# Kernel tuning notes

Measured on AMD Instinct MI355X. Metric: run time of the kernel, lower is better.

The kernel has to match this reference:

```python
import jax, jax.numpy as jnp
import numpy as np

SIMILARITY_EPS = 1e-4
B, N, M, K = 4096, 16384, 12, 2048  # batch, signal length, n ref spectra, spectrum bins


def setup_inputs() -> dict:
    key = jax.random.key(0)
    k1, k2, k3 = jax.random.split(key, 3)
    Y = jax.random.normal(k1, (B, N), dtype=jnp.float32)
    model_spectra = jax.random.uniform(k2, (M, K), dtype=jnp.float32)
    dissonance_vals = jax.random.uniform(k3, (M,), dtype=jnp.float32)
    return {"Y": Y, "model_spectra": model_spectra, "dissonance_vals": dissonance_vals}


def reference(Y, model_spectra, dissonance_vals):
    n = Y.shape[-1]
    k = model_spectra.shape[-1]
    # FFT magnitude spectrum, scaled, truncated to first K bins: [B, K]
    yf = (2.0 / n) * jnp.abs(jnp.fft.fft(Y, axis=-1)[:, :k])
    # Euclidean distance to each reference spectrum via expansion (avoids [B,M,K] intermediate)
    sq = (jnp.sum(yf * yf, axis=-1, keepdims=True)            # [B,1]
          + jnp.sum(model_spectra * model_spectra, axis=-1)   # [M]
          - 2.0 * (yf @ model_spectra.T))                     # [B,M]
    dist = jnp.sqrt(jnp.maximum(sq, 0.0))                     # [B,M]
    sim = 1.0 / (dist + SIMILARITY_EPS)                       # [B,M]
    w = sim / jnp.sum(sim, axis=-1, keepdims=True)            # [B,M]
    out = w @ (1.0 - dissonance_vals)                         # [B]
    return out[:, None]                                       # [B,1]
```

## Files before the change

### kernel.cpp

```cpp
#include <hip/hip_runtime.h>
#include <hip/hip_bf16.h>
#include <math.h>

#define BATCH 4096
#define NSIG  16384
#define MREF  12
#define KBIN  2048

constexpr float SIM_EPS = 1e-4f;
constexpr float TWO_PI = 6.2831853071795864769f;

typedef __attribute__((ext_vector_type(8))) short bfrag;
typedef __attribute__((ext_vector_type(4))) float f32x4;
typedef __attribute__((ext_vector_type(4))) int   i32x4;
typedef __attribute__((ext_vector_type(4))) unsigned u32x4;

__device__ unsigned g_wtab[16 * 256 * 4];
__device__ unsigned g_b2tab[1024 * 4];
__device__ unsigned g_utw[32 * 128 * 4];
__device__ float    g_msn[MREF];

__device__ inline unsigned short f2bf(float x) {
  unsigned u = __builtin_bit_cast(unsigned, x);
  u += 0x7fffu + ((u >> 16) & 1u);
  return (unsigned short)(u >> 16);
}
__device__ inline unsigned pkbf(float lo, float hi) {
  return (unsigned)f2bf(lo) | ((unsigned)f2bf(hi) << 16);
}
__device__ inline float bflo(unsigned u) { return __builtin_bit_cast(float, u << 16); }
__device__ inline float bfhi(unsigned u) { return __builtin_bit_cast(float, u & 0xffff0000u); }
__device__ inline f32x4 mfma16(bfrag a, bfrag b, f32x4 c) {
  return __builtin_amdgcn_mfma_f32_16x16x32_bf16(a, b, c, 0, 0, 0);
}

__global__ __launch_bounds__(256) void setup_kernel(const float* __restrict__ ms) {
  const int blk = blockIdx.x, t = threadIdx.x;
  if (blk < 16) {
    const int ri = blk & 1, ks = (blk >> 1) & 3, mt = blk >> 3;
    const int lane = t & 63, w = t >> 6, c = lane & 15, g = lane >> 4;
    const int k1 = 32 * w + 16 * mt + c;
    unsigned wd[4];
    #pragma unroll
    for (int jp = 0; jp < 4; ++jp) {
      float v[2];
      #pragma unroll
      for (int h = 0; h < 2; ++h) {
        const int n1 = 32 * ks + 8 * g + 2 * jp + h;
        const float th = TWO_PI * (float)((k1 * n1) & 127) / 128.f;
        float sn, cs; sincosf(th, &sn, &cs);
        v[h] = ri ? -sn : cs;
      }
      wd[jp] = pkbf(v[0], v[1]);
    }
    *(u32x4*)&g_wtab[(blk * 256 + t) * 4] = (u32x4){wd[0], wd[1], wd[2], wd[3]};
  } else if (blk == 16) {
    #pragma unroll
    for (int r = 0; r < 4; ++r) {
      const int e = t * 4 + r;
      const int lane = e & 63, ri = (e >> 6) & 1, s_ = (e >> 7) & 1, ch = (e >> 8) & 3;
      const int c = lane & 15, g = lane >> 4;
      unsigned wd[4];
      #pragma unroll
      for (int i = 0; i < 4; ++i) {
        const int ang = (c * (32 * ch + 16 * s_ + 4 * g + i)) & 127;
        const float th = TWO_PI * (float)ang / 128.f;
        float sn, cs; sincosf(th, &sn, &cs);
        wd[i] = ri ? pkbf(-sn, cs) : pkbf(cs, sn);
      }
      *(u32x4*)&g_b2tab[e * 4] = (u32x4){wd[0], wd[1], wd[2], wd[3]};
    }
  } else if (blk < 25) {
    const int base = (blk - 17) * 512 + t;
    #pragma unroll
    for (int r = 0; r < 2; ++r) {
      const int e = base + r * 256;
      const int a = e >> 7, n2 = e & 127;
      unsigned wd[4];
      #pragma unroll
      for (int q = 0; q < 4; ++q) {
        const int ang = ((4 * a + q) * n2) & 16383;
        const float th = TWO_PI * (float)ang / 16384.f;
        float sn, cs; sincosf(th, &sn, &cs);
        wd[q] = pkbf(cs, -sn);
      }
      *(u32x4*)&g_utw[e * 4] = (u32x4){wd[0], wd[1], wd[2], wd[3]};
    }
  } else {
    const int m = blk - 25;
    if (m < MREF) {
      float p = 0.f;
      for (int i = t; i < KBIN; i += 256) { float v = ms[m * KBIN + i]; p += v * v; }
      #pragma unroll
      for (int o = 32; o; o >>= 1) p += __shfl_xor(p, o, 64);
      __shared__ float r4[4];
      if ((t & 63) == 0) r4[t >> 6] = p;
      __syncthreads();
      if (t == 0) g_msn[m] = r4[0] + r4[1] + r4[2] + r4[3];
    }
  }
}

__global__ __launch_bounds__(256, 2) void consonance_kernel(
    const float* __restrict__ Y, const float* __restrict__ ms,
    const float* __restrict__ diss, float* __restrict__ out) {
  __shared__ __align__(16) unsigned short Ysb[128 * 128];
  __shared__ __align__(16) unsigned Ua[4 * 32 * 32];
  __shared__ float red[4][13];

  const int t = threadIdx.x;
  const int b = blockIdx.x;
  const int lane = t & 63;
  const int w = t >> 6;
  const int g = lane >> 4;
  const int c = lane & 15;

  {
    const int c0 = (t & 31) << 2;
    const int h  = t >> 5;
    const float* yrow = Y + (size_t)b * NSIG + c0;
    float4 v[16];
    #pragma unroll
    for (int r = 0; r < 16; ++r)
      v[r] = *(const float4*)(yrow + 128 * (16 * h + r));
    #pragma unroll
    for (int u = 0; u < 2; ++u) {
      #pragma unroll
      for (int cc = 0; cc < 4; ++cc) {
        const int n2 = c0 + cc;
        unsigned p0 = pkbf((&v[8*u+0].x)[cc], (&v[8*u+1].x)[cc]);
        unsigned p1 = pkbf((&v[8*u+2].x)[cc], (&v[8*u+3].x)[cc]);
        unsigned p2 = pkbf((&v[8*u+4].x)[cc], (&v[8*u+5].x)[cc]);
        unsigned p3 = pkbf((&v[8*u+6].x)[cc], (&v[8*u+7].x)[cc]);
        const int blk = (2 * h + u) ^ (n2 & 7);
        *(i32x4*)((char*)Ysb + n2 * 256 + (blk << 4)) =
            (i32x4){(int)p0, (int)p1, (int)p2, (int)p3};
      }
    }
  }

  bfrag Wr[2][4], Wi[2][4];
  #pragma unroll
  for (int mt = 0; mt < 2; ++mt)
    #pragma unroll
    for (int ks = 0; ks < 4; ++ks) {
      Wr[mt][ks] = *(const bfrag*)&g_wtab[(((mt * 4 + ks) * 2 + 0) * 256 + t) * 4];
      Wi[mt][ks] = *(const bfrag*)&g_wtab[(((mt * 4 + ks) * 2 + 1) * 256 + t) * 4];
    }

  f32x4 aXr[2] = {{0.f,0.f,0.f,0.f},{0.f,0.f,0.f,0.f}};
  f32x4 aXi[2] = {{0.f,0.f,0.f,0.f},{0.f,0.f,0.f,0.f}};
  unsigned* uw = Ua + (w << 10);

  __syncthreads();

  #pragma unroll 1
  for (int ch = 0; ch < 4; ++ch) {
    bfrag bfr[2][4];
    #pragma unroll
    for (int nt = 0; nt < 2; ++nt) {
      const int n2 = 32 * ch + 16 * nt + c;
      #pragma unroll
      for (int ks = 0; ks < 4; ++ks) {
        const int blk = (4 * ks + g) ^ (n2 & 7);
        bfr[nt][ks] = *(const bfrag*)((const char*)Ysb + n2 * 256 + (blk << 4));
      }
    }
    f32x4 aTr[2][2] = {{{0.f,0.f,0.f,0.f},{0.f,0.f,0.f,0.f}},
                       {{0.f,0.f,0.f,0.f},{0.f,0.f,0.f,0.f}}};
    f32x4 aTi[2][2] = {{{0.f,0.f,0.f,0.f},{0.f,0.f,0.f,0.f}},
                       {{0.f,0.f,0.f,0.f},{0.f,0.f,0.f,0.f}}};
    #pragma unroll
    for (int mt = 0; mt < 2; ++mt)
      #pragma unroll
      for (int nt = 0; nt < 2; ++nt)
        #pragma unroll
        for (int ks = 0; ks < 4; ++ks) {
          aTr[mt][nt] = mfma16(Wr[mt][ks], bfr[nt][ks], aTr[mt][nt]);
          aTi[mt][nt] = mfma16(Wi[mt][ks], bfr[nt][ks], aTi[mt][nt]);
        }
    #pragma unroll
    for (int nt = 0; nt < 2; ++nt) {
      const int n2 = 32 * ch + 16 * nt + c;
      #pragma unroll
      for (int mt = 0; mt < 2; ++mt) {
        const int a = 8 * w + 4 * mt + g;
        const u32x4 tw = *(const u32x4*)&g_utw[(a * 128 + n2) * 4];
        #pragma unroll
        for (int q = 0; q < 4; ++q) {
          const float twr = bflo(tw[q]), twi = bfhi(tw[q]);
          const float tr = aTr[mt][nt][q], ti = aTi[mt][nt][q];
          const float ur = tr * twr - ti * twi;
          const float ui = tr * twi + ti * twr;
          const int rl = 16 * mt + 4 * g + q;
          const int tt = 16 * nt + c;
          uw[rl * 32 + (tt ^ ((rl & 7) << 2))] = pkbf(ur, ui);
        }
      }
    }
    bfrag B2[2][2];
    #pragma unroll
    for (int s = 0; s < 2; ++s) {
      B2[0][s] = *(const bfrag*)&g_b2tab[(((ch * 2 + s) * 2 + 0) * 64 + lane) * 4];
      B2[1][s] = *(const bfrag*)&g_b2tab[(((ch * 2 + s) * 2 + 1) * 64 + lane) * 4];
    }
    #pragma unroll
    for (int mt = 0; mt < 2; ++mt) {
      const int rl = 16 * mt + c;
      #pragma unroll
      for (int s = 0; s < 2; ++s) {
        const int t4 = (16 * s + 4 * g) ^ ((rl & 7) << 2);
        bfrag af = *(const bfrag*)((const char*)uw + rl * 128 + (t4 << 2));
        aXr[mt] = mfma16(af, B2[0][s], aXr[mt]);
        aXi[mt] = mfma16(af, B2[1][s], aXi[mt]);
      }
    }
  }

  const float scale = 2.0f / (float)NSIG;
  float yfv[2][4], S = 0.f;
  #pragma unroll
  for (int mt = 0; mt < 2; ++mt)
    #pragma unroll
    for (int q = 0; q < 4; ++q) {
      const float xr = aXr[mt][q], xi = aXi[mt][q];
      const float yf = scale * sqrtf(xr * xr + xi * xi);
      yfv[mt][q] = yf;
      S += yf * yf;
    }
  float dot[MREF];
  #pragma unroll
  for (int m = 0; m < MREF; ++m) dot[m] = 0.f;
  const int kb0 = 32 * w + 4 * g + 128 * c;
  #pragma unroll
  for (int m = 0; m < MREF; ++m) {
    #pragma unroll
    for (int mt = 0; mt < 2; ++mt) {
      const float4 mv = *(const float4*)&ms[m * KBIN + kb0 + 16 * mt];
      dot[m] = fmaf(yfv[mt][0], mv.x, dot[m]);
      dot[m] = fmaf(yfv[mt][1], mv.y, dot[m]);
      dot[m] = fmaf(yfv[mt][2], mv.z, dot[m]);
      dot[m] = fmaf(yfv[mt][3], mv.w, dot[m]);
    }
  }
  #pragma unroll
  for (int o = 32; o; o >>= 1) {
    S += __shfl_xor(S, o, 64);
    #pragma unroll
    for (int m = 0; m < MREF; ++m) dot[m] += __shfl_xor(dot[m], o, 64);
  }
  if (lane == 0) {
    red[w][0] = S;
    #pragma unroll
    for (int m = 0; m < MREF; ++m) red[w][1 + m] = dot[m];
  }
  __syncthreads();
  if (t == 0) {
    const float St = red[0][0] + red[1][0] + red[2][0] + red[3][0];
    float ssum = 0.f, wsum = 0.f;
    for (int m = 0; m < MREF; ++m) {
      const float dm = red[0][1 + m] + red[1][1 + m] + red[2][1 + m] + red[3][1 + m];
      const float d2 = St + g_msn[m] - 2.f * dm;
      const float dist = sqrtf(fmaxf(d2, 0.f));
      const float sim = 1.f / (dist + SIM_EPS);
      ssum += sim;
      wsum += sim * (1.f - diss[m]);
    }
    out[b] = wsum / ssum;
  }
}

extern "C" void kernel_launch(void* const* d_in, const int* in_sizes, int n_in,
                              void* d_out, int out_size, void* d_ws, size_t ws_size,
                              hipStream_t stream) {
  const float* Y    = (const float*)d_in[0];
  const float* ms   = (const float*)d_in[1];
  const float* diss = (const float*)d_in[2];
  float* outp = (float*)d_out;
  setup_kernel<<<37, 256, 0, stream>>>(ms);
  consonance_kernel<<<BATCH, 256, 0, stream>>>(Y, ms, diss, outp);
}
```

Before: 435.8 us.

## Prefetch twiddles, use hardware bf16 pack, raise occupancy, fix LDS swizzle

Switches bf16 packing to the v_cvt_pk_bf16_f32 instruction instead of manual rounding. It raises launch bounds to 4 blocks per CU and splits the Y load into two halves to cut register pressure. Twiddle and W table loads are hoisted and software-prefetched one chunk ahead, and the chunk loop is fully unrolled. The LDS swizzle now mixes in higher row bits to reduce bank conflicts. Forcing 4 waves/SIMD may cause register spills, and the LDS footprint (~49KB per block) may cap occupancy anyway.

```diff
diff --git a/kernel.cpp b/kernel.cpp
--- a/kernel.cpp
+++ b/kernel.cpp
@@ -20,19 +20,17 @@
 __device__ unsigned g_utw[32 * 128 * 4];
 __device__ float    g_msn[MREF];
 
-__device__ inline unsigned short f2bf(float x) {
-  unsigned u = __builtin_bit_cast(unsigned, x);
-  u += 0x7fffu + ((u >> 16) & 1u);
-  return (unsigned short)(u >> 16);
-}
 __device__ inline unsigned pkbf(float lo, float hi) {
-  return (unsigned)f2bf(lo) | ((unsigned)f2bf(hi) << 16);
+  unsigned r;
+  asm("v_cvt_pk_bf16_f32 %0, %1, %2" : "=v"(r) : "v"(lo), "v"(hi));
+  return r;
 }
 __device__ inline float bflo(unsigned u) { return __builtin_bit_cast(float, u << 16); }
 __device__ inline float bfhi(unsigned u) { return __builtin_bit_cast(float, u & 0xffff0000u); }
 __device__ inline f32x4 mfma16(bfrag a, bfrag b, f32x4 c) {
   return __builtin_amdgcn_mfma_f32_16x16x32_bf16(a, b, c, 0, 0, 0);
 }
+__device__ inline int fsw(int n2) { return (n2 ^ (n2 >> 2)) & 7; }
 
 __global__ __launch_bounds__(256) void setup_kernel(const float* __restrict__ ms) {
   const int blk = blockIdx.x, t = threadIdx.x;
@@ -101,7 +99,7 @@
   }
 }
 
-__global__ __launch_bounds__(256, 2) void consonance_kernel(
+__global__ __launch_bounds__(256, 4) void consonance_kernel(
     const float* __restrict__ Y, const float* __restrict__ ms,
     const float* __restrict__ diss, float* __restrict__ out) {
   __shared__ __align__(16) unsigned short Ysb[128 * 128];
@@ -115,38 +113,46 @@
   const int g = lane >> 4;
   const int c = lane & 15;
 
+  bfrag Wr[2][4], Wi[2][4];
+  #pragma unroll
+  for (int mt = 0; mt < 2; ++mt)
+    #pragma unroll
+    for (int ks = 0; ks < 4; ++ks) {
+      Wr[mt][ks] = *(const bfrag*)&g_wtab[(((mt * 4 + ks) * 2 + 0) * 256 + t) * 4];
+      Wi[mt][ks] = *(const bfrag*)&g_wtab[(((mt * 4 + ks) * 2 + 1) * 256 + t) * 4];
+    }
+  u32x4 utwP[2][2];
+  #pragma unroll
+  for (int nt = 0; nt < 2; ++nt)
+    #pragma unroll
+    for (int mt = 0; mt < 2; ++mt) {
+      const int a = 8 * w + 4 * mt + g;
+      utwP[nt][mt] = *(const u32x4*)&g_utw[(a * 128 + (16 * nt + c)) * 4];
+    }
+
   {
     const int c0 = (t & 31) << 2;
     const int h  = t >> 5;
     const float* yrow = Y + (size_t)b * NSIG + c0;
-    float4 v[16];
-    #pragma unroll
-    for (int r = 0; r < 16; ++r)
-      v[r] = *(const float4*)(yrow + 128 * (16 * h + r));
     #pragma unroll
     for (int u = 0; u < 2; ++u) {
+      float4 v[8];
+      #pragma unroll
+      for (int r = 0; r < 8; ++r)
+        v[r] = *(const float4*)(yrow + 128 * (16 * h + 8 * u + r));
       #pragma unroll
       for (int cc = 0; cc < 4; ++cc) {
         const int n2 = c0 + cc;
-        unsigned p0 = pkbf((&v[8*u+0].x)[cc], (&v[8*u+1].x)[cc]);
-        unsigned p1 = pkbf((&v[8*u+2].x)[cc], (&v[8*u+3].x)[cc]);
-        unsigned p2 = pkbf((&v[8*u+4].x)[cc], (&v[8*u+5].x)[cc]);
-        unsigned p3 = pkbf((&v[8*u+6].x)[cc], (&v[8*u+7].x)[cc]);
-        const int blk = (2 * h + u) ^ (n2 & 7);
+        unsigned p0 = pkbf((&v[0].x)[cc], (&v[1].x)[cc]);
+        unsigned p1 = pkbf((&v[2].x)[cc], (&v[3].x)[cc]);
+        unsigned p2 = pkbf((&v[4].x)[cc], (&v[5].x)[cc]);
+        unsigned p3 = pkbf((&v[6].x)[cc], (&v[7].x)[cc]);
+        const int blk = (2 * h + u) ^ fsw(n2);
         *(i32x4*)((char*)Ysb + n2 * 256 + (blk << 4)) =
             (i32x4){(int)p0, (int)p1, (int)p2, (int)p3};
       }
     }
   }
-
-  bfrag Wr[2][4], Wi[2][4];
-  #pragma unroll
-  for (int mt = 0; mt < 2; ++mt)
-    #pragma unroll
-    for (int ks = 0; ks < 4; ++ks) {
-      Wr[mt][ks] = *(const bfrag*)&g_wtab[(((mt * 4 + ks) * 2 + 0) * 256 + t) * 4];
-      Wi[mt][ks] = *(const bfrag*)&g_wtab[(((mt * 4 + ks) * 2 + 1) * 256 + t) * 4];
-    }
 
   f32x4 aXr[2] = {{0.f,0.f,0.f,0.f},{0.f,0.f,0.f,0.f}};
   f32x4 aXi[2] = {{0.f,0.f,0.f,0.f},{0.f,0.f,0.f,0.f}};
@@ -154,15 +160,35 @@
 
   __syncthreads();
 
-  #pragma unroll 1
+  #pragma unroll
   for (int ch = 0; ch < 4; ++ch) {
+    bfrag B2[2][2];
+    #pragma unroll
+    for (int s = 0; s < 2; ++s) {
+      B2[0][s] = *(const bfrag*)&g_b2tab[(((ch * 2 + s) * 2 + 0) * 64 + lane) * 4];
+      B2[1][s] = *(const bfrag*)&g_b2tab[(((ch * 2 + s) * 2 + 1) * 64 + lane) * 4];
+    }
+    u32x4 utwC[2][2];
+    #pragma unroll
+    for (int nt = 0; nt < 2; ++nt)
+      #pragma unroll
+      for (int mt = 0; mt < 2; ++mt) utwC[nt][mt] = utwP[nt][mt];
+    if (ch < 3) {
+      #pragma unroll
+      for (int nt = 0; nt < 2; ++nt)
+        #pragma unroll
+        for (int mt = 0; mt < 2; ++mt) {
+          const int a = 8 * w + 4 * mt + g;
+          utwP[nt][mt] = *(const u32x4*)&g_utw[(a * 128 + (32 * (ch + 1) + 16 * nt + c)) * 4];
+        }
+    }
     bfrag bfr[2][4];
     #pragma unroll
     for (int nt = 0; nt < 2; ++nt) {
       const int n2 = 32 * ch + 16 * nt + c;
       #pragma unroll
       for (int ks = 0; ks < 4; ++ks) {
-        const int blk = (4 * ks + g) ^ (n2 & 7);
+        const int blk = (4 * ks + g) ^ fsw(n2);
         bfr[nt][ks] = *(const bfrag*)((const char*)Ysb + n2 * 256 + (blk << 4));
       }
     }
@@ -181,11 +207,9 @@
         }
     #pragma unroll
     for (int nt = 0; nt < 2; ++nt) {
-      const int n2 = 32 * ch + 16 * nt + c;
       #pragma unroll
       for (int mt = 0; mt < 2; ++mt) {
-        const int a = 8 * w + 4 * mt + g;
-        const u32x4 tw = *(const u32x4*)&g_utw[(a * 128 + n2) * 4];
+        const u32x4 tw = utwC[nt][mt];
         #pragma unroll
         for (int q = 0; q < 4; ++q) {
           const float twr = bflo(tw[q]), twi = bfhi(tw[q]);
@@ -197,12 +221,6 @@
           uw[rl * 32 + (tt ^ ((rl & 7) << 2))] = pkbf(ur, ui);
         }
       }
-    }
-    bfrag B2[2][2];
-    #pragma unroll
-    for (int s = 0; s < 2; ++s) {
-      B2[0][s] = *(const bfrag*)&g_b2tab[(((ch * 2 + s) * 2 + 0) * 64 + lane) * 4];
-      B2[1][s] = *(const bfrag*)&g_b2tab[(((ch * 2 + s) * 2 + 1) * 64 + lane) * 4];
     }
     #pragma unroll
     for (int mt = 0; mt < 2; ++mt) {
```

New measurement: 420.5 us. 3.5% less time.
